# Kernel optimization log

Hardware: AMD Instinct MI355X
Metric: run time of the kernel (lower is better)

The kernel has to match this reference:

```python
import jax, jax.numpy as jnp
import numpy as np
import itertools

GRID_SIZES = [0.01, 0.02, 0.04, 0.08, 0.16, 0.32, 0.64, 1.28]
OFFSETS = np.array(list(itertools.product([-1, 0, 1], repeat=3)), dtype=np.int32)  # [27,3]; index 13 = (0,0,0)
B, N, IN_DIM, HID, OUT_DIM = 2, 65536, 3, 32, 128


def make_neighbors(p, g):
    """Submanifold-conv neighbor tables for one grid scale.
    Returns nbr [27, b*n] int32 (flat point id or -1) and mask [27, b*n] bool.
    """
    b, n, _ = p.shape
    D = int(np.ceil(1.0 / g)) + 1  # static upper bound on spatial shape (p in [0,1))
    gc = jnp.floor(p / g).astype(jnp.int32)
    gc = gc - jnp.min(gc, axis=1, keepdims=True)  # per-batch min, as in torch code
    ids = jnp.arange(b * n, dtype=jnp.int32).reshape(b, n)
    bidx = jnp.arange(b, dtype=jnp.int32)[:, None]
    # deterministic voxel hash: one representative point id per occupied voxel
    grid = jnp.full((b, D, D, D), -1, jnp.int32)
    grid = grid.at[bidx, gc[..., 0], gc[..., 1], gc[..., 2]].max(ids)
    off = jnp.asarray(OFFSETS)
    nc = gc[None] + off[:, None, None, :]  # [27,b,n,3]
    valid = jnp.all((nc >= 0) & (nc < D), axis=-1)
    ncc = jnp.clip(nc, 0, D - 1)
    nbr = grid[bidx[None], ncc[..., 0], ncc[..., 1], ncc[..., 2]]  # [27,b,n]
    mask = valid & (nbr >= 0)
    nbr = nbr.at[13].set(ids)  # center tap is always the point itself
    mask = mask.at[13].set(True)
    return nbr.reshape(27, b * n), mask.reshape(27, b * n)


def subm_conv(f, W, bias, nbr, mask):
    """Submanifold 3x3x3 sparse conv on active sites.
    f [M,h]; W [27,h,h]; nbr/mask [27,M]. out[p] = bias + sum_k (f @ W_k)[nbr_k(p)] (masked).
    Scan over the 27 kernel taps keeps peak memory at O(M*h).
    """
    def step(acc, kin):
        Wk, nbrk, mk = kin
        acc = acc + jnp.where(mk[:, None], (f @ Wk)[nbrk], 0.0)
        return acc, None
    acc0 = jnp.zeros_like(f) + bias
    out, _ = jax.lax.scan(step, acc0, (W, nbr, mask))
    return out


def mssc_forward(p, w1, b1, w_mlp, b_mlp, w_conv, b_conv, w2, b2, neighbors):
    b, n, _ = p.shape
    pts = p @ w1 + b1  # mlp_1: [b,n,HID]
    outs = []
    for i in range(len(GRID_SIZES)):
        nbr, mask = neighbors[i]
        h0 = (pts @ w_mlp[i] + b_mlp[i]).reshape(b * n, HID)  # per-scale MLP
        h1 = subm_conv(h0, w_conv[2 * i], b_conv[2 * i], nbr, mask) + h0
        h2 = subm_conv(h1, w_conv[2 * i + 1], b_conv[2 * i + 1], nbr, mask) + h1
        outs.append(h2 + h0)  # features + features_batch residual
    feat = jnp.concatenate(outs, axis=1).reshape(b, n, HID * len(GRID_SIZES))
    return feat @ w2 + b2  # mlp_2


def setup_inputs():
    key = jax.random.key(0)
    ks = jax.random.split(key, 10)
    L = len(GRID_SIZES)
    return {
        "p": jax.random.uniform(ks[0], (B, N, IN_DIM), jnp.float32),
        "w1": jax.random.normal(ks[1], (IN_DIM, HID), jnp.float32) / np.sqrt(IN_DIM),
        "b1": 0.01 * jax.random.normal(ks[2], (HID,), jnp.float32),
        "w_mlp": jax.random.normal(ks[3], (L, HID, HID), jnp.float32) / np.sqrt(HID),
        "b_mlp": 0.01 * jax.random.normal(ks[4], (L, HID), jnp.float32),
        "w_conv": jax.random.normal(ks[5], (2 * L, 27, HID, HID), jnp.float32) / np.sqrt(27 * HID),
        "b_conv": 0.01 * jax.random.normal(ks[6], (2 * L, HID), jnp.float32),
        "w2": jax.random.normal(ks[7], (HID * L, OUT_DIM), jnp.float32) / np.sqrt(HID * L),
        "b2": 0.01 * jax.random.normal(ks[8], (OUT_DIM,), jnp.float32),
    }


def reference(p, w1, b1, w_mlp, b_mlp, w_conv, b_conv, w2, b2):
    neighbors = [make_neighbors(p, g) for g in GRID_SIZES]
    return mssc_forward(p, w1, b1, w_mlp, b_mlp, w_conv, b_conv, w2, b2, neighbors)
```

## Files before the change

### kernel.cpp

```cpp
#include <hip/hip_runtime.h>

#define MTOT 131072
#define NB   65536
#define SNBINS 265302
#define SNB_BLOCKS 1037

typedef __attribute__((ext_vector_type(8))) __bf16 bf16x8;
typedef __attribute__((ext_vector_type(4))) __bf16 bf16x4;
typedef __attribute__((ext_vector_type(4))) float  f32x4;

__global__ void pmin_init_kernel(float* pmin){
    if (threadIdx.x < 6) pmin[threadIdx.x] = 2.0f;
}

__global__ void pmin_kernel(const float* __restrict__ p, float* __restrict__ pmin){
    int bi = blockIdx.y;
    float m0 = 2.f, m1 = 2.f, m2 = 2.f;
    for (int ni = blockIdx.x * blockDim.x + threadIdx.x; ni < NB; ni += gridDim.x * blockDim.x){
        const float* pp = p + ((size_t)bi * NB + ni) * 3;
        m0 = fminf(m0, pp[0]); m1 = fminf(m1, pp[1]); m2 = fminf(m2, pp[2]);
    }
    #pragma unroll
    for (int o = 32; o > 0; o >>= 1){
        m0 = fminf(m0, __shfl_down(m0, o, 64));
        m1 = fminf(m1, __shfl_down(m1, o, 64));
        m2 = fminf(m2, __shfl_down(m2, o, 64));
    }
    if ((threadIdx.x & 63) == 0){
        atomicMin((int*)(pmin + bi*3 + 0), __float_as_int(m0));
        atomicMin((int*)(pmin + bi*3 + 1), __float_as_int(m1));
        atomicMin((int*)(pmin + bi*3 + 2), __float_as_int(m2));
    }
}

__device__ __forceinline__ int sort_bin(const float* __restrict__ p, int m){
    int bi = m >> 16;
    int gx = (int)(p[m*3+0] * 51.0f); gx = gx > 50 ? 50 : gx;
    int gy = (int)(p[m*3+1] * 51.0f); gy = gy > 50 ? 50 : gy;
    int gz = (int)(p[m*3+2] * 51.0f); gz = gz > 50 ? 50 : gz;
    return bi * 132651 + (gx * 51 + gy) * 51 + gz;
}

__global__ void shist_kernel(const float* __restrict__ p, int* __restrict__ hist){
    int m = blockIdx.x * 256 + threadIdx.x;
    atomicAdd(hist + sort_bin(p, m), 1);
}

__global__ void sscan1_kernel(const int* __restrict__ hist, int* __restrict__ offs,
                              int* __restrict__ bsum){
    __shared__ int sh[256];
    int tid = threadIdx.x;
    int idx = blockIdx.x * 256 + tid;
    int v = (idx < SNBINS) ? hist[idx] : 0;
    sh[tid] = v;
    __syncthreads();
    #pragma unroll
    for (int off = 1; off < 256; off <<= 1){
        int t = (tid >= off) ? sh[tid - off] : 0;
        __syncthreads();
        sh[tid] += t;
        __syncthreads();
    }
    if (idx < SNBINS) offs[idx] = sh[tid] - v;
    if (tid == 255) bsum[blockIdx.x] = sh[255];
}

__global__ void sscan2_kernel(int* __restrict__ bsum){
    __shared__ int sh[256];
    int tid = threadIdx.x;
    const int CH = (SNB_BLOCKS + 255) / 256;
    int base = tid * CH, sum = 0;
    #pragma unroll
    for (int i = 0; i < CH; i++){
        int idx = base + i;
        if (idx < SNB_BLOCKS) sum += bsum[idx];
    }
    sh[tid] = sum;
    __syncthreads();
    #pragma unroll
    for (int off = 1; off < 256; off <<= 1){
        int t = (tid >= off) ? sh[tid - off] : 0;
        __syncthreads();
        sh[tid] += t;
        __syncthreads();
    }
    int run = (tid == 0) ? 0 : sh[tid - 1];
    #pragma unroll
    for (int i = 0; i < CH; i++){
        int idx = base + i;
        if (idx < SNB_BLOCKS){ int v = bsum[idx]; bsum[idx] = run; run += v; }
    }
}

__global__ void sscan3_kernel(int* __restrict__ offs, const int* __restrict__ bsum){
    int idx = blockIdx.x * 256 + threadIdx.x;
    if (idx < SNBINS) offs[idx] += bsum[blockIdx.x];
}

__global__ void sscatter_kernel(const float* __restrict__ p, int* __restrict__ offs,
                                int* __restrict__ sortpos, int* __restrict__ origid){
    int m = blockIdx.x * 256 + threadIdx.x;
    int pos = atomicAdd(offs + sort_bin(p, m), 1);
    sortpos[m] = pos;
    origid[pos] = m;
}

template<int USE_LDS>
__global__ void scatter_kernel(const float* __restrict__ p, const float* __restrict__ pmin,
                               int* __restrict__ vgrid, int* __restrict__ gcbuf,
                               double gd, int D){
    extern __shared__ int lgrid[];
    int m  = blockIdx.x * blockDim.x + threadIdx.x;
    int bi = m >> 16;
    double px = (double)p[m*3], py = (double)p[m*3+1], pz = (double)p[m*3+2];
    int gx = (int)floor(px / gd) - (int)floor((double)pmin[bi*3+0] / gd);
    int gy = (int)floor(py / gd) - (int)floor((double)pmin[bi*3+1] / gd);
    int gz = (int)floor(pz / gd) - (int)floor((double)pmin[bi*3+2] / gd);
    gcbuf[m] = (gx << 20) | (gy << 10) | gz;
    int cell = (gx * D + gy) * D + gz;

    if (!USE_LDS){
        atomicMax(vgrid + bi * D * D * D + cell, m);
        return;
    }
    int ncell = D * D * D;
    for (int c = threadIdx.x; c < ncell; c += 256) lgrid[c] = -1;
    __syncthreads();
    atomicMax(&lgrid[cell], m);
    __syncthreads();
    int* vg = vgrid + bi * ncell;
    for (int c = threadIdx.x; c < ncell; c += 256){
        int v = lgrid[c];
        if (v >= 0) atomicMax(vg + c, v);
    }
}

__global__ void nbr_kernel(const int* __restrict__ gcbuf, const int* __restrict__ vgrid,
                           const int* __restrict__ origid, const int* __restrict__ sortpos,
                           int* __restrict__ nbr, int D){
    int s  = blockIdx.x * blockDim.x + threadIdx.x;
    int m  = origid ? origid[s] : s;
    int bi = m >> 16;
    int pk = gcbuf[m];
    int gx = pk >> 20, gy = (pk >> 10) & 1023, gz = pk & 1023;
    #pragma unroll
    for (int k = 0; k < 27; k++){
        int v;
        if (k == 13){
            v = s;
        } else {
            int x = gx + (k/9) - 1;
            int y = gy + ((k/3)%3) - 1;
            int z = gz + (k%3) - 1;
            if (x < 0 || y < 0 || z < 0 || x >= D || y >= D || z >= D) v = -1;
            else {
                v = vgrid[((bi * D + x) * D + y) * D + z];
                if (v >= 0 && sortpos) v = sortpos[v];
            }
        }
        nbr[k * MTOT + s] = v;
    }
}

__global__ void nbrv_kernel(const int* __restrict__ vgrid, const int* __restrict__ sortpos,
                            int* __restrict__ nbrv, int D, int NC2, int NC2pad){
    int ci = blockIdx.x * 256 + threadIdx.x;
    if (ci >= NC2pad) return;
    int D3 = D * D * D;
    int bi = (ci >= D3) ? 1 : 0;
    int r  = ci - bi * D3;
    int x = r / (D*D), y = (r / D) % D, z = r % D;
    #pragma unroll
    for (int k = 0; k < 27; k++){
        int v = -1;
        if (ci < NC2){
            int nx = x + (k/9) - 1;
            int ny = y + ((k/3)%3) - 1;
            int nz = z + (k%3) - 1;
            if (nx >= 0 && ny >= 0 && nz >= 0 && nx < D && ny < D && nz < D){
                v = vgrid[bi * D3 + ((nx * D + ny) * D + nz)];
                if (v >= 0 && sortpos) v = sortpos[v];
            }
        }
        nbrv[k * NC2pad + ci] = v;
    }
}

__global__ void wcv_wave_kernel(const float* __restrict__ w_conv,
                                __bf16* __restrict__ wth, __bf16* __restrict__ wtl){
    int o = blockIdx.x * 256 + threadIdx.x;
    int cv = o / 27648, r = o % 27648;
    int k = r / 1024, q = r % 1024;
    int half = q >> 9, t = q & 511;
    int l = t >> 3, e = t & 7;
    int c = half*16 + (l & 15);
    int j = (l >> 4)*8 + e;
    float x = w_conv[cv*27648 + k*1024 + j*32 + c];
    __bf16 hi = (__bf16)x;
    wth[o] = hi;
    wtl[o] = (__bf16)(x - (float)hi);
}

__global__ void wcv_kernel(const float* __restrict__ w_conv,
                           __bf16* __restrict__ wth, __bf16* __restrict__ wtl){
    int o = blockIdx.x * 256 + threadIdx.x;
    int cv = o / 27648, r = o % 27648;
    int k = r / 1024, q = r % 1024, c = q / 32, j = q % 32;
    float x = w_conv[cv*27648 + k*1024 + j*32 + c];
    __bf16 hi = (__bf16)x;
    wth[o] = hi;
    wtl[o] = (__bf16)(x - (float)hi);
}

__global__ void w2t_kernel(const float* __restrict__ w2,
                           __bf16* __restrict__ w2th, __bf16* __restrict__ w2tl){
    int o = blockIdx.x * 256 + threadIdx.x;
    int kc = o >> 12, r = o & 4095, c = r >> 5, j = r & 31;
    float x = w2[(kc*32 + j)*128 + c];
    __bf16 hi = (__bf16)x;
    w2th[o] = hi;
    w2tl[o] = (__bf16)(x - (float)hi);
}

__global__ void mlp_scale_kernel(const float* __restrict__ p, const int* __restrict__ origid,
                                 const float* __restrict__ w1, const float* __restrict__ b1,
                                 const float* __restrict__ w, const float* __restrict__ b,
                                 __bf16* __restrict__ h0h, __bf16* __restrict__ h0l){
    int t = blockIdx.x * blockDim.x + threadIdx.x;
    int c = t & 31, s = t >> 5;
    int m = origid ? origid[s] : s;
    float x = p[m*3+0], y = p[m*3+1], z = p[m*3+2];
    float acc = b[c];
    #pragma unroll
    for (int j = 0; j < 32; j++){
        float ptsj = b1[j] + x * w1[j] + y * w1[32 + j] + z * w1[64 + j];
        acc += ptsj * w[j*32 + c];
    }
    __bf16 hi = (__bf16)acc;
    h0h[t] = hi;
    h0l[t] = (__bf16)(acc - (float)hi);
}

template<int MODE>
__global__ __launch_bounds__(256)
void conv4_kernel(const __bf16* __restrict__ fh, const __bf16* __restrict__ fl,
                  const __bf16* __restrict__ wth, const __bf16* __restrict__ wtl,
                  const float* __restrict__ bias, const int* __restrict__ nbr,
                  const __bf16* __restrict__ r2h, const __bf16* __restrict__ r2l,
                  __bf16* __restrict__ outh, __bf16* __restrict__ outl)
{
    __shared__ float buf0[32][33], buf1[32][33];
    int tid  = threadIdx.x;
    int lane = tid & 63, w = tid >> 6;
    int col  = lane & 15, kq = lane >> 4;
    int ptA  = blockIdx.x * 32 + col, ptB = ptA + 16;
    const int fragoff = kq * 8;

    f32x4 acc00, acc01, acc10, acc11;
    if (w == 0){
        float bv0 = bias[col], bv1 = bias[col + 16];
        acc00 = (f32x4){bv0,bv0,bv0,bv0}; acc01 = (f32x4){bv1,bv1,bv1,bv1};
        acc10 = (f32x4){bv0,bv0,bv0,bv0}; acc11 = (f32x4){bv1,bv1,bv1,bv1};
    } else {
        acc00 = (f32x4){0,0,0,0}; acc01 = (f32x4){0,0,0,0};
        acc10 = (f32x4){0,0,0,0}; acc11 = (f32x4){0,0,0,0};
    }

    int k0 = w * 7, k1 = (k0 + 7 < 27) ? k0 + 7 : 27;

    int idc = nbr[k0 * MTOT + ptA];
    int jdc = nbr[k0 * MTOT + ptB];
    int idn = (k0 + 1 < k1) ? nbr[(k0+1) * MTOT + ptA] : 0;
    int jdn = (k0 + 1 < k1) ? nbr[(k0+1) * MTOT + ptB] : 0;
    size_t oc0 = (size_t)(idc < 0 ? 0 : idc) * 32 + fragoff;
    size_t oc1 = (size_t)(jdc < 0 ? 0 : jdc) * 32 + fragoff;
    bf16x8 a0h = *(const bf16x8*)(fh + oc0);
    bf16x8 a0l = *(const bf16x8*)(fl + oc0);
    bf16x8 a1h = *(const bf16x8*)(fh + oc1);
    bf16x8 a1l = *(const bf16x8*)(fl + oc1);
    bool mc0 = idc < 0, mc1 = jdc < 0;

    #pragma unroll 1
    for (int k = k0; k < k1; k++){
        int idn2 = 0, jdn2 = 0;
        if (k + 2 < k1){ idn2 = nbr[(k+2) * MTOT + ptA]; jdn2 = nbr[(k+2) * MTOT + ptB]; }
        size_t on0 = (size_t)(idn < 0 ? 0 : idn) * 32 + fragoff;
        size_t on1 = (size_t)(jdn < 0 ? 0 : jdn) * 32 + fragoff;
        bf16x8 na0h = *(const bf16x8*)(fh + on0);
        bf16x8 na0l = *(const bf16x8*)(fl + on0);
        bf16x8 na1h = *(const bf16x8*)(fh + on1);
        bf16x8 na1l = *(const bf16x8*)(fl + on1);
        bool nm0 = idn < 0, nm1 = jdn < 0;

        const __bf16* wb = wth + (size_t)k*1024 + lane*8;
        const __bf16* wc = wtl + (size_t)k*1024 + lane*8;
        bf16x8 b0h = *(const bf16x8*)(wb);
        bf16x8 b1h = *(const bf16x8*)(wb + 512);
        bf16x8 b0l = *(const bf16x8*)(wc);
        bf16x8 b1l = *(const bf16x8*)(wc + 512);

        bf16x8 z = {};
        bf16x8 xa0h = mc0 ? z : a0h, xa0l = mc0 ? z : a0l;
        bf16x8 xa1h = mc1 ? z : a1h, xa1l = mc1 ? z : a1l;

        acc00 = __builtin_amdgcn_mfma_f32_16x16x32_bf16(xa0h, b0h, acc00, 0,0,0);
        acc00 = __builtin_amdgcn_mfma_f32_16x16x32_bf16(xa0h, b0l, acc00, 0,0,0);
        acc00 = __builtin_amdgcn_mfma_f32_16x16x32_bf16(xa0l, b0h, acc00, 0,0,0);
        acc01 = __builtin_amdgcn_mfma_f32_16x16x32_bf16(xa0h, b1h, acc01, 0,0,0);
        acc01 = __builtin_amdgcn_mfma_f32_16x16x32_bf16(xa0h, b1l, acc01, 0,0,0);
        acc01 = __builtin_amdgcn_mfma_f32_16x16x32_bf16(xa0l, b1h, acc01, 0,0,0);
        acc10 = __builtin_amdgcn_mfma_f32_16x16x32_bf16(xa1h, b0h, acc10, 0,0,0);
        acc10 = __builtin_amdgcn_mfma_f32_16x16x32_bf16(xa1h, b0l, acc10, 0,0,0);
        acc10 = __builtin_amdgcn_mfma_f32_16x16x32_bf16(xa1l, b0h, acc10, 0,0,0);
        acc11 = __builtin_amdgcn_mfma_f32_16x16x32_bf16(xa1h, b1h, acc11, 0,0,0);
// ... 154 lines not shown
        acc00 = __builtin_amdgcn_mfma_f32_16x16x32_bf16(xa0h, b0h, acc00, 0,0,0);
        acc00 = __builtin_amdgcn_mfma_f32_16x16x32_bf16(xa0h, b0l, acc00, 0,0,0);
        acc00 = __builtin_amdgcn_mfma_f32_16x16x32_bf16(xa0l, b0h, acc00, 0,0,0);
        acc01 = __builtin_amdgcn_mfma_f32_16x16x32_bf16(xa0h, b1h, acc01, 0,0,0);
        acc01 = __builtin_amdgcn_mfma_f32_16x16x32_bf16(xa0h, b1l, acc01, 0,0,0);
        acc01 = __builtin_amdgcn_mfma_f32_16x16x32_bf16(xa0l, b1h, acc01, 0,0,0);
        acc10 = __builtin_amdgcn_mfma_f32_16x16x32_bf16(xa1h, b0h, acc10, 0,0,0);
        acc10 = __builtin_amdgcn_mfma_f32_16x16x32_bf16(xa1h, b0l, acc10, 0,0,0);
        acc10 = __builtin_amdgcn_mfma_f32_16x16x32_bf16(xa1l, b0h, acc10, 0,0,0);
        acc11 = __builtin_amdgcn_mfma_f32_16x16x32_bf16(xa1h, b1h, acc11, 0,0,0);
        acc11 = __builtin_amdgcn_mfma_f32_16x16x32_bf16(xa1h, b1l, acc11, 0,0,0);
        acc11 = __builtin_amdgcn_mfma_f32_16x16x32_bf16(xa1l, b1h, acc11, 0,0,0);

        a0h = na0h; a0l = na0l; a1h = na1h; a1l = na1l;
        mc0 = nm0; mc1 = nm1; idn = idn2; jdn = jdn2;
    }

    if (w == 2){
        #pragma unroll
        for (int r = 0; r < 4; r++){
            buf0[kq*4 + r][col]           = acc00[r];
            buf0[kq*4 + r][col + 16]      = acc01[r];
            buf0[16 + kq*4 + r][col]      = acc10[r];
            buf0[16 + kq*4 + r][col + 16] = acc11[r];
        }
    } else if (w == 3){
        #pragma unroll
        for (int r = 0; r < 4; r++){
            buf1[kq*4 + r][col]           = acc00[r];
            buf1[kq*4 + r][col + 16]      = acc01[r];
            buf1[16 + kq*4 + r][col]      = acc10[r];
            buf1[16 + kq*4 + r][col + 16] = acc11[r];
        }
    }
    __syncthreads();
    if (w == 0){
        #pragma unroll
        for (int r = 0; r < 4; r++){
            acc00[r] += buf0[kq*4 + r][col];
            acc01[r] += buf0[kq*4 + r][col + 16];
            acc10[r] += buf0[16 + kq*4 + r][col];
            acc11[r] += buf0[16 + kq*4 + r][col + 16];
        }
    } else if (w == 1){
        #pragma unroll
        for (int r = 0; r < 4; r++){
            acc00[r] += buf1[kq*4 + r][col];
            acc01[r] += buf1[kq*4 + r][col + 16];
            acc10[r] += buf1[16 + kq*4 + r][col];
            acc11[r] += buf1[16 + kq*4 + r][col + 16];
        }
    }
    __syncthreads();
    if (w == 1){
        #pragma unroll
        for (int r = 0; r < 4; r++){
            buf1[kq*4 + r][col]           = acc00[r];
            buf1[kq*4 + r][col + 16]      = acc01[r];
            buf1[16 + kq*4 + r][col]      = acc10[r];
            buf1[16 + kq*4 + r][col + 16] = acc11[r];
        }
    }
    __syncthreads();
    if (w == 0){
        #pragma unroll
        for (int r = 0; r < 4; r++){
            buf0[kq*4 + r][col]           = acc00[r] + buf1[kq*4 + r][col];
            buf0[kq*4 + r][col + 16]      = acc01[r] + buf1[kq*4 + r][col + 16];
            buf0[16 + kq*4 + r][col]      = acc10[r] + buf1[16 + kq*4 + r][col];
            buf0[16 + kq*4 + r][col + 16] = acc11[r] + buf1[16 + kq*4 + r][col + 16];
        }
    }
    __syncthreads();

    int pt = tid >> 3, c0 = (tid & 7) * 4;
    float* o = vv + (size_t)(blockIdx.x * 32 + pt) * 32 + c0;
    ((float4*)o)[0] = make_float4(buf0[pt][c0], buf0[pt][c0+1], buf0[pt][c0+2], buf0[pt][c0+3]);
}

template<int MODE>
__global__ __launch_bounds__(256)
void combine_kernel(const __bf16* __restrict__ fh, const __bf16* __restrict__ fl,
                    const __bf16* __restrict__ wth, const __bf16* __restrict__ wtl,
                    const float* __restrict__ vv, const int* __restrict__ gcbuf,
                    const int* __restrict__ origid, int D,
                    const __bf16* __restrict__ r2h, const __bf16* __restrict__ r2l,
                    __bf16* __restrict__ outh, __bf16* __restrict__ outl)
{
    __shared__ float vsh[128][33];
    int tid  = threadIdx.x;
    int lane = tid & 63, w = tid >> 6;
    int col  = lane & 15, kq = lane >> 4;
    const int fragoff = kq * 8;
    int mB  = blockIdx.x * 128 + w * 32;
    int ptA = mB + col, ptB = ptA + 16;

    size_t oA = (size_t)ptA * 32 + fragoff;
    size_t oB = (size_t)ptB * 32 + fragoff;
    bf16x8 a0h = *(const bf16x8*)(fh + oA);
    bf16x8 a0l = *(const bf16x8*)(fl + oA);
    bf16x8 a1h = *(const bf16x8*)(fh + oB);
    bf16x8 a1l = *(const bf16x8*)(fl + oB);

    const __bf16* wb = wth + 13*1024 + lane*8;
    const __bf16* wc = wtl + 13*1024 + lane*8;
    bf16x8 b0h = *(const bf16x8*)(wb);
    bf16x8 b1h = *(const bf16x8*)(wb + 512);
    bf16x8 b0l = *(const bf16x8*)(wc);
    bf16x8 b1l = *(const bf16x8*)(wc + 512);

    f32x4 acc00 = {0,0,0,0}, acc01 = {0,0,0,0}, acc10 = {0,0,0,0}, acc11 = {0,0,0,0};
    acc00 = __builtin_amdgcn_mfma_f32_16x16x32_bf16(a0h, b0h, acc00, 0,0,0);
    acc00 = __builtin_amdgcn_mfma_f32_16x16x32_bf16(a0h, b0l, acc00, 0,0,0);
    acc00 = __builtin_amdgcn_mfma_f32_16x16x32_bf16(a0l, b0h, acc00, 0,0,0);
    acc01 = __builtin_amdgcn_mfma_f32_16x16x32_bf16(a0h, b1h, acc01, 0,0,0);
    acc01 = __builtin_amdgcn_mfma_f32_16x16x32_bf16(a0h, b1l, acc01, 0,0,0);
    acc01 = __builtin_amdgcn_mfma_f32_16x16x32_bf16(a0l, b1h, acc01, 0,0,0);
    acc10 = __builtin_amdgcn_mfma_f32_16x16x32_bf16(a1h, b0h, acc10, 0,0,0);
    acc10 = __builtin_amdgcn_mfma_f32_16x16x32_bf16(a1h, b0l, acc10, 0,0,0);
    acc10 = __builtin_amdgcn_mfma_f32_16x16x32_bf16(a1l, b0h, acc10, 0,0,0);
    acc11 = __builtin_amdgcn_mfma_f32_16x16x32_bf16(a1h, b1h, acc11, 0,0,0);
    acc11 = __builtin_amdgcn_mfma_f32_16x16x32_bf16(a1h, b1l, acc11, 0,0,0);
    acc11 = __builtin_amdgcn_mfma_f32_16x16x32_bf16(a1l, b1h, acc11, 0,0,0);

    #pragma unroll
    for (int r = 0; r < 4; r++){
        vsh[w*32 + kq*4 + r][col]           = acc00[r];
        vsh[w*32 + kq*4 + r][col + 16]      = acc01[r];
        vsh[w*32 + 16 + kq*4 + r][col]      = acc10[r];
        vsh[w*32 + 16 + kq*4 + r][col + 16] = acc11[r];
    }
    __syncthreads();

    int pt = tid >> 1, c0 = (tid & 1) * 16;
    int s  = blockIdx.x * 128 + pt;
    int m  = origid ? origid[s] : s;
    int pk = gcbuf[m];
    int bi = m >> 16;
    int gx = pk >> 20, gy = (pk >> 10) & 1023, gz = pk & 1023;
    int ci = ((bi * D + gx) * D + gy) * D + gz;

    const float* vrow = vv + (size_t)ci * 32 + c0;
    size_t g = (size_t)s * 32 + c0;
    bf16x8 rh0 = *(const bf16x8*)(fh + g);
    bf16x8 rh1 = *(const bf16x8*)(fh + g + 8);
    bf16x8 rl0 = *(const bf16x8*)(fl + g);
    bf16x8 rl1 = *(const bf16x8*)(fl + g + 8);
    bf16x8 sh0, sh1, sl0, sl1;
    if (MODE == 1){
        sh0 = *(const bf16x8*)(r2h + g);
        sh1 = *(const bf16x8*)(r2h + g + 8);
        sl0 = *(const bf16x8*)(r2l + g);
        sl1 = *(const bf16x8*)(r2l + g + 8);
    }
    bf16x8 oh0, oh1, ol0, ol1;
    #pragma unroll
    for (int j = 0; j < 8; j++){
        float v = vsh[pt][c0 + j] + vrow[j] + (float)rh0[j] + (float)rl0[j];
        if (MODE == 1) v += (float)sh0[j] + (float)sl0[j];
        __bf16 hi = (__bf16)v;
        oh0[j] = hi; ol0[j] = (__bf16)(v - (float)hi);
    }
    #pragma unroll
    for (int j = 0; j < 8; j++){
        float v = vsh[pt][c0 + 8 + j] + vrow[8 + j] + (float)rh1[j] + (float)rl1[j];
        if (MODE == 1) v += (float)sh1[j] + (float)sl1[j];
        __bf16 hi = (__bf16)v;
        oh1[j] = hi; ol1[j] = (__bf16)(v - (float)hi);
    }
    *(bf16x8*)(outh + g)     = oh0;
    *(bf16x8*)(outh + g + 8) = oh1;
    *(bf16x8*)(outl + g)     = ol0;
    *(bf16x8*)(outl + g + 8) = ol1;
}

__global__ __launch_bounds__(256)
void mlp2_kernel(const __bf16* __restrict__ vplanes,
                 const __bf16* __restrict__ w2th, const __bf16* __restrict__ w2tl,
                 const float* __restrict__ b2, const int* __restrict__ origid,
                 float* __restrict__ out)
{
    int tid  = threadIdx.x;
    int lane = tid & 63, w = tid >> 6;
    int col  = lane & 15, kq = lane >> 4;
    const int fragoff = kq * 8;
    int pbase = blockIdx.x * 128 + w * 32;
    size_t oA = (size_t)(pbase + col) * 32 + fragoff;
    size_t oB = (size_t)(pbase + 16 + col) * 32 + fragoff;

    f32x4 acc[4][4];
    #pragma unroll
    for (int s = 0; s < 4; s++)
        #pragma unroll
        for (int q = 0; q < 4; q++) acc[s][q] = (f32x4){0,0,0,0};

    bf16x8 a0h = *(const bf16x8*)(vplanes + oA);
    bf16x8 a0l = *(const bf16x8*)(vplanes + 4194304 + oA);
    bf16x8 a1h = *(const bf16x8*)(vplanes + oB);
    bf16x8 a1l = *(const bf16x8*)(vplanes + 4194304 + oB);

    #pragma unroll 1
    for (int kc = 0; kc < 8; kc++){
        bf16x8 na0h, na0l, na1h, na1l;
        if (kc < 7){
            const __bf16* fnh = vplanes + (size_t)(kc+1) * 8388608;
            const __bf16* fnl = fnh + 4194304;
            na0h = *(const bf16x8*)(fnh + oA);
            na0l = *(const bf16x8*)(fnl + oA);
            na1h = *(const bf16x8*)(fnh + oB);
            na1l = *(const bf16x8*)(fnl + oB);
        } else {
            na0h = a0h; na0l = a0l; na1h = a1h; na1l = a1l;
        }

        const __bf16* wbase  = w2th + (size_t)kc * 4096;
        const __bf16* wlbase = w2tl + (size_t)kc * 4096;
        #pragma unroll
        for (int s = 0; s < 4; s++){
            const __bf16* wb = wbase  + (s*32 + col) * 32 + fragoff;
            const __bf16* wc = wlbase + (s*32 + col) * 32 + fragoff;
            bf16x8 b0h = *(const bf16x8*)(wb);
            bf16x8 b1h = *(const bf16x8*)(wb + 512);
            bf16x8 b0l = *(const bf16x8*)(wc);
            bf16x8 b1l = *(const bf16x8*)(wc + 512);

            acc[s][0] = __builtin_amdgcn_mfma_f32_16x16x32_bf16(a0h, b0h, acc[s][0], 0,0,0);
            acc[s][0] = __builtin_amdgcn_mfma_f32_16x16x32_bf16(a0h, b0l, acc[s][0], 0,0,0);
            acc[s][0] = __builtin_amdgcn_mfma_f32_16x16x32_bf16(a0l, b0h, acc[s][0], 0,0,0);
            acc[s][1] = __builtin_amdgcn_mfma_f32_16x16x32_bf16(a0h, b1h, acc[s][1], 0,0,0);
            acc[s][1] = __builtin_amdgcn_mfma_f32_16x16x32_bf16(a0h, b1l, acc[s][1], 0,0,0);
            acc[s][1] = __builtin_amdgcn_mfma_f32_16x16x32_bf16(a0l, b1h, acc[s][1], 0,0,0);
            acc[s][2] = __builtin_amdgcn_mfma_f32_16x16x32_bf16(a1h, b0h, acc[s][2], 0,0,0);
            acc[s][2] = __builtin_amdgcn_mfma_f32_16x16x32_bf16(a1h, b0l, acc[s][2], 0,0,0);
            acc[s][2] = __builtin_amdgcn_mfma_f32_16x16x32_bf16(a1l, b0h, acc[s][2], 0,0,0);
            acc[s][3] = __builtin_amdgcn_mfma_f32_16x16x32_bf16(a1h, b1h, acc[s][3], 0,0,0);
            acc[s][3] = __builtin_amdgcn_mfma_f32_16x16x32_bf16(a1h, b1l, acc[s][3], 0,0,0);
            acc[s][3] = __builtin_amdgcn_mfma_f32_16x16x32_bf16(a1l, b1h, acc[s][3], 0,0,0);
        }

        a0h = na0h; a0l = na0l; a1h = na1h; a1l = na1l;
    }

    #pragma unroll
    for (int s = 0; s < 4; s++){
        float bl = b2[s*32 + col], bh = b2[s*32 + 16 + col];
        #pragma unroll
        for (int r = 0; r < 4; r++){
            int iA = pbase + kq*4 + r;
            int iB = pbase + 16 + kq*4 + r;
            size_t rowA = (size_t)(origid ? origid[iA] : iA) * 128;
            size_t rowB = (size_t)(origid ? origid[iB] : iB) * 128;
            out[rowA + s*32 + col]      = acc[s][0][r] + bl;
            out[rowA + s*32 + 16 + col] = acc[s][1][r] + bh;
            out[rowB + s*32 + col]      = acc[s][2][r] + bl;
            out[rowB + s*32 + 16 + col] = acc[s][3][r] + bh;
        }
    }
}

template<int MODE>
__global__ __launch_bounds__(256)
void conv_mfma_kernel(const __bf16* __restrict__ fh, const __bf16* __restrict__ fl,
                      const __bf16* __restrict__ wth, const __bf16* __restrict__ wtl,
                      const float* __restrict__ bias, const int* __restrict__ nbr,
                      const __bf16* __restrict__ r2h, const __bf16* __restrict__ r2l,
                      const float* __restrict__ w2i, const float* __restrict__ b2,
                      __bf16* __restrict__ outh, __bf16* __restrict__ outl,
                      float* __restrict__ out)
{
    __shared__ float vsh[64][33];
    int tid  = threadIdx.x;
    int lane = tid & 63, wid = tid >> 6;
    int pair = wid >> 1;
    int half = wid & 1;
    int col  = lane & 15, kq = lane >> 4;
    int m0   = blockIdx.x * 64 + pair * 32;
    int ptA  = m0 + col, ptB = ptA + 16;
    const int fragoff = kq * 8;

    f32x4 acc00, acc01, acc10, acc11;
    if (half == 0){
        float bv0 = bias[col], bv1 = bias[col + 16];
        acc00 = (f32x4){bv0,bv0,bv0,bv0}; acc01 = (f32x4){bv1,bv1,bv1,bv1};
        acc10 = (f32x4){bv0,bv0,bv0,bv0}; acc11 = (f32x4){bv1,bv1,bv1,bv1};
    } else {
        acc00 = (f32x4){0,0,0,0}; acc01 = (f32x4){0,0,0,0};
        acc10 = (f32x4){0,0,0,0}; acc11 = (f32x4){0,0,0,0};
    }

    int k0 = half ? 14 : 0;
    int k1 = half ? 27 : 14;
    #pragma unroll 1
    for (int k = k0; k < k1; k++){
        int nb0 = nbr[k * MTOT + ptA];
        int nb1 = nbr[k * MTOT + ptB];
        size_t o0 = (size_t)(nb0 < 0 ? 0 : nb0) * 32 + fragoff;
        size_t o1 = (size_t)(nb1 < 0 ? 0 : nb1) * 32 + fragoff;
        bf16x8 a0h = *(const bf16x8*)(fh + o0);
        bf16x8 a0l = *(const bf16x8*)(fl + o0);
        bf16x8 a1h = *(const bf16x8*)(fh + o1);
        bf16x8 a1l = *(const bf16x8*)(fl + o1);
        bf16x8 z = {};
        if (nb0 < 0){ a0h = z; a0l = z; }
        if (nb1 < 0){ a1h = z; a1l = z; }

        const __bf16* wb = wth + (size_t)k*1024 + col*32 + fragoff;
        const __bf16* wc = wtl + (size_t)k*1024 + col*32 + fragoff;
        bf16x8 b0h = *(const bf16x8*)(wb);
        bf16x8 b1h = *(const bf16x8*)(wb + 512);
        bf16x8 b0l = *(const bf16x8*)(wc);
        bf16x8 b1l = *(const bf16x8*)(wc + 512);

        acc00 = __builtin_amdgcn_mfma_f32_16x16x32_bf16(a0h, b0h, acc00, 0,0,0);
        acc00 = __builtin_amdgcn_mfma_f32_16x16x32_bf16(a0h, b0l, acc00, 0,0,0);
        acc00 = __builtin_amdgcn_mfma_f32_16x16x32_bf16(a0l, b0h, acc00, 0,0,0);
        acc01 = __builtin_amdgcn_mfma_f32_16x16x32_bf16(a0h, b1h, acc01, 0,0,0);
        acc01 = __builtin_amdgcn_mfma_f32_16x16x32_bf16(a0h, b1l, acc01, 0,0,0);
        acc01 = __builtin_amdgcn_mfma_f32_16x16x32_bf16(a0l, b1h, acc01, 0,0,0);
        acc10 = __builtin_amdgcn_mfma_f32_16x16x32_bf16(a1h, b0h, acc10, 0,0,0);
        acc10 = __builtin_amdgcn_mfma_f32_16x16x32_bf16(a1h, b0l, acc10, 0,0,0);
        acc10 = __builtin_amdgcn_mfma_f32_16x16x32_bf16(a1l, b0h, acc10, 0,0,0);
        acc11 = __builtin_amdgcn_mfma_f32_16x16x32_bf16(a1h, b1h, acc11, 0,0,0);
        acc11 = __builtin_amdgcn_mfma_f32_16x16x32_bf16(a1h, b1l, acc11, 0,0,0);
        acc11 = __builtin_amdgcn_mfma_f32_16x16x32_bf16(a1l, b1h, acc11, 0,0,0);
    }

    if (half == 1){
        #pragma unroll
        for (int r = 0; r < 4; r++){
            vsh[pair*32 + kq*4 + r][col]           = acc00[r];
            vsh[pair*32 + kq*4 + r][col + 16]      = acc01[r];
            vsh[pair*32 + 16 + kq*4 + r][col]      = acc10[r];
            vsh[pair*32 + 16 + kq*4 + r][col + 16] = acc11[r];
        }
    }
    __syncthreads();
    if (half == 0){
        #pragma unroll
// ... 20 lines not shown
            oh8[j] = hi;
            ol8[j] = (__bf16)(v - (float)hi);
        }
        *(bf16x8*)(outh + g) = oh8;
        *(bf16x8*)(outl + g) = ol8;
    } else {
        int eidx = tid * 8;
        int pt = eidx >> 5, c0 = eidx & 31;
        size_t g = (size_t)blockIdx.x * 2048 + eidx;
        bf16x8 rh = *(const bf16x8*)(fh + g);
        bf16x8 rl = *(const bf16x8*)(fl + g);
        bf16x8 sh = *(const bf16x8*)(r2h + g);
        bf16x8 sl = *(const bf16x8*)(r2l + g);
        #pragma unroll
        for (int j = 0; j < 8; j++)
            vsh[pt][c0 + j] += (float)rh[j] + (float)rl[j] + (float)sh[j] + (float)sl[j];
        __syncthreads();

        int pm = tid & 63;
        int tg = __builtin_amdgcn_readfirstlane(tid >> 6);
        size_t m = (size_t)blockIdx.x * 64 + pm;
        float o32[32];
        float* obase = out + m*128 + tg*32;
        if (MODE == 2){
            #pragma unroll
            for (int o = 0; o < 32; o++) o32[o] = b2[tg*32 + o];
        } else {
            #pragma unroll
            for (int q = 0; q < 8; q++){
                float4 t4 = ((const float4*)obase)[q];
                o32[q*4+0] = t4.x; o32[q*4+1] = t4.y; o32[q*4+2] = t4.z; o32[q*4+3] = t4.w;
            }
        }
        #pragma unroll
        for (int c = 0; c < 32; c++){
            float vc = vsh[pm][c];
            const float* w2r = w2i + c*128 + tg*32;
            #pragma unroll
            for (int o = 0; o < 32; o++) o32[o] += vc * w2r[o];
        }
        #pragma unroll
        for (int q = 0; q < 8; q++)
            ((float4*)obase)[q] = make_float4(o32[q*4+0], o32[q*4+1], o32[q*4+2], o32[q*4+3]);
    }
}

extern "C" void kernel_launch(void* const* d_in, const int* in_sizes, int n_in,
                              void* d_out, int out_size, void* d_ws, size_t ws_size,
                              hipStream_t stream)
{
    static const int want[9] = {393216, 96, 32, 8192, 256, 442368, 512, 32768, 128};
    const void* bound[9];
    for (int i = 0; i < 9; i++) bound[i] = d_in[i];
    if (n_in == 9){
        for (int i = 0; i < 9; i++)
            for (int j = 0; j < 9; j++)
                if (in_sizes[j] == want[i]) { bound[i] = d_in[j]; break; }
    }
    const float* p      = (const float*)bound[0];
    const float* w1     = (const float*)bound[1];
    const float* b1     = (const float*)bound[2];
    const float* w_mlp  = (const float*)bound[3];
    const float* b_mlp  = (const float*)bound[4];
    const float* w_conv = (const float*)bound[5];
    const float* b_conv = (const float*)bound[6];
    const float* w2     = (const float*)bound[7];
    const float* b2     = (const float*)bound[8];
    float* out = (float*)d_out;

    char* ws = (char*)d_ws;
    __bf16* h0h  = (__bf16*)(ws);
    __bf16* h0l  = (__bf16*)(ws + 8388608);
    __bf16* h1h  = (__bf16*)(ws + 16777216);
    int*    vgrid= (int*)   (ws + 16777216);
    __bf16* h1l  = (__bf16*)(ws + 25165824);
    int*    nbr  = (int*)   (ws + 33554432);
    int*    nbrv = (int*)   (ws + 33554432);
    float*  vv   = (float*) (ws + 33554432 + 6291456);
    __bf16* wth  = (__bf16*)(ws + 47710208);
    __bf16* wtl  = (__bf16*)(ws + 48594944);
    __bf16* w2th = (__bf16*)(ws + 49479680);
    __bf16* w2tl = (__bf16*)(ws + 49545216);
    float*  pmin = (float*) (ws + 49610752);
    int*    gcbuf= (int*)   (ws + 49612800);
    __bf16* vpl  = (__bf16*)(ws + 50331648);
    int*    hist = (int*)   (ws + 184549376);
    int*    offs = (int*)   (ws + 185614336);
    int*    sortpos=(int*)  (ws + 186679296);
    int*    origid =(int*)  (ws + 187203584);
    int*    bsum   =(int*)  (ws + 187727872);

    const bool big = (ws_size >= 184549376ULL);
    const bool srt = (ws_size >= 187736064ULL);
    const int* oid = srt ? origid  : nullptr;
    const int* spp = srt ? sortpos : nullptr;

    static const double GS[8] = {0.01, 0.02, 0.04, 0.08, 0.16, 0.32, 0.64, 1.28};
    static const int    DS[8] = {101, 51, 26, 14, 8, 5, 3, 2};

    pmin_init_kernel<<<1, 64, 0, stream>>>(pmin);
    pmin_kernel<<<dim3(64, 2), 256, 0, stream>>>(p, pmin);
    if (big){
        wcv_wave_kernel<<<1728, 256, 0, stream>>>(w_conv, wth, wtl);
        w2t_kernel<<<128, 256, 0, stream>>>(w2, w2th, w2tl);
    } else {
        wcv_kernel<<<1728, 256, 0, stream>>>(w_conv, wth, wtl);
    }
    if (srt){
        hipMemsetAsync(hist, 0, SNBINS*sizeof(int), stream);
        shist_kernel<<<MTOT/256, 256, 0, stream>>>(p, hist);
        sscan1_kernel<<<SNB_BLOCKS, 256, 0, stream>>>(hist, offs, bsum);
        sscan2_kernel<<<1, 256, 0, stream>>>(bsum);
        sscan3_kernel<<<SNB_BLOCKS, 256, 0, stream>>>(offs, bsum);
        sscatter_kernel<<<MTOT/256, 256, 0, stream>>>(p, offs, sortpos, origid);
    }

    for (int i = 0; i < 8; i++){
        int D = DS[i]; double gd = GS[i];
        int ncell = D * D * D;
        int NC2 = 2 * ncell;
        hipMemsetAsync(vgrid, 0xFF, (size_t)NC2*sizeof(int), stream);
        if (ncell <= 2744)
            scatter_kernel<1><<<MTOT/256, 256, ncell*sizeof(int), stream>>>(p, pmin, vgrid, gcbuf, gd, D);
        else
            scatter_kernel<0><<<MTOT/256, 256, 0, stream>>>(p, pmin, vgrid, gcbuf, gd, D);

        const bool voxel = big && (NC2 < MTOT);

        if (voxel){
            int NC2pad = (NC2 + 31) & ~31;
            nbrv_kernel<<<(NC2pad + 255)/256, 256, 0, stream>>>(vgrid, spp, nbrv, D, NC2, NC2pad);
            mlp_scale_kernel<<<(MTOT*32)/256, 256, 0, stream>>>(
                p, oid, w1, b1, w_mlp + i*1024, b_mlp + i*32, h0h, h0l);
            vconv_kernel<<<NC2pad/32, 256, 0, stream>>>(
                h0h, h0l, wth + (size_t)(2*i)*27648, wtl + (size_t)(2*i)*27648,
                b_conv + (2*i)*32, nbrv, NC2pad, vv);
            combine_kernel<0><<<MTOT/128, 256, 0, stream>>>(
                h0h, h0l, wth + (size_t)(2*i)*27648, wtl + (size_t)(2*i)*27648,
                vv, gcbuf, oid, D, nullptr, nullptr, h1h, h1l);
            vconv_kernel<<<NC2pad/32, 256, 0, stream>>>(
                h1h, h1l, wth + (size_t)(2*i+1)*27648, wtl + (size_t)(2*i+1)*27648,
                b_conv + (2*i+1)*32, nbrv, NC2pad, vv);
            combine_kernel<1><<<MTOT/128, 256, 0, stream>>>(
                h1h, h1l, wth + (size_t)(2*i+1)*27648, wtl + (size_t)(2*i+1)*27648,
                vv, gcbuf, oid, D, h0h, h0l,
                vpl + (size_t)i*8388608, vpl + (size_t)i*8388608 + 4194304);
        } else {
            nbr_kernel<<<MTOT/256, 256, 0, stream>>>(gcbuf, vgrid, oid, spp, nbr, D);
            mlp_scale_kernel<<<(MTOT*32)/256, 256, 0, stream>>>(
                p, oid, w1, b1, w_mlp + i*1024, b_mlp + i*32, h0h, h0l);
            if (big){
                conv4_kernel<0><<<MTOT/32, 256, 0, stream>>>(
                    h0h, h0l, wth + (size_t)(2*i)*27648, wtl + (size_t)(2*i)*27648,
                    b_conv + (2*i)*32, nbr, nullptr, nullptr, h1h, h1l);
                conv4_kernel<1><<<MTOT/32, 256, 0, stream>>>(
                    h1h, h1l, wth + (size_t)(2*i+1)*27648, wtl + (size_t)(2*i+1)*27648,
                    b_conv + (2*i+1)*32, nbr, h0h, h0l,
                    vpl + (size_t)i*8388608, vpl + (size_t)i*8388608 + 4194304);
            } else {
                conv_mfma_kernel<0><<<MTOT/64, 256, 0, stream>>>(
                    h0h, h0l, wth + (size_t)(2*i)*27648, wtl + (size_t)(2*i)*27648,
                    b_conv + (2*i)*32, nbr, nullptr, nullptr, nullptr, nullptr,
                    h1h, h1l, nullptr);
                if (i == 0)
                    conv_mfma_kernel<2><<<MTOT/64, 256, 0, stream>>>(
                        h1h, h1l, wth + (size_t)(2*i+1)*27648, wtl + (size_t)(2*i+1)*27648,
                        b_conv + (2*i+1)*32, nbr, h0h, h0l, w2 + i*32*128, b2,
                        nullptr, nullptr, out);
                else
                    conv_mfma_kernel<1><<<MTOT/64, 256, 0, stream>>>(
                        h1h, h1l, wth + (size_t)(2*i+1)*27648, wtl + (size_t)(2*i+1)*27648,
                        b_conv + (2*i+1)*32, nbr, h0h, h0l, w2 + i*32*128, nullptr,
                        nullptr, nullptr, out);
            }
        }
    }
    if (big)
        mlp2_kernel<<<MTOT/128, 256, 0, stream>>>(vpl, w2th, w2tl, b2, oid, out);
}
```

Measured before the change: 887.2 us.

## Store coordinates and points in sorted order; translate voxel grid once; halve mlp2 tile

Writes the packed voxel coordinates (now carrying the batch bit) and a sorted copy of the point positions directly in sorted order. A small per-scale kernel remaps the voxel grid to sorted ids once, so the neighbor and combine kernels no longer do indirect origid/sortpos lookups per tap. The mlp2 kernel now handles 64 points per block instead of 128, which doubles the grid and lowers register use per wave. This costs an extra pass over the grid at each scale and a larger workspace requirement; if the workspace is too small, the sorted path is disabled.

Result: no change. 900.6 us (+1.5%).

```diff
diff --git a/kernel.cpp b/kernel.cpp
--- a/kernel.cpp
+++ b/kernel.cpp
@@ -98,16 +98,21 @@
 }
 
 __global__ void sscatter_kernel(const float* __restrict__ p, int* __restrict__ offs,
-                                int* __restrict__ sortpos, int* __restrict__ origid){
+                                int* __restrict__ sortpos, int* __restrict__ origid,
+                                float* __restrict__ ps){
     int m = blockIdx.x * 256 + threadIdx.x;
     int pos = atomicAdd(offs + sort_bin(p, m), 1);
     sortpos[m] = pos;
     origid[pos] = m;
+    ps[pos*3+0] = p[m*3+0];
+    ps[pos*3+1] = p[m*3+1];
+    ps[pos*3+2] = p[m*3+2];
 }
 
 template<int USE_LDS>
 __global__ void scatter_kernel(const float* __restrict__ p, const float* __restrict__ pmin,
-                               int* __restrict__ vgrid, int* __restrict__ gcbuf,
+                               const int* __restrict__ sortpos,
+                               int* __restrict__ vgrid, int* __restrict__ gcs,
                                double gd, int D){
     extern __shared__ int lgrid[];
     int m  = blockIdx.x * blockDim.x + threadIdx.x;
@@ -116,7 +121,8 @@
     int gx = (int)floor(px / gd) - (int)floor((double)pmin[bi*3+0] / gd);
     int gy = (int)floor(py / gd) - (int)floor((double)pmin[bi*3+1] / gd);
     int gz = (int)floor(pz / gd) - (int)floor((double)pmin[bi*3+2] / gd);
-    gcbuf[m] = (gx << 20) | (gy << 10) | gz;
+    int pos = sortpos ? sortpos[m] : m;
+    gcs[pos] = (bi << 30) | (gx << 20) | (gy << 10) | gz;
     int cell = (gx * D + gy) * D + gz;
 
     if (!USE_LDS){
@@ -135,14 +141,19 @@
     }
 }
 
-__global__ void nbr_kernel(const int* __restrict__ gcbuf, const int* __restrict__ vgrid,
-                           const int* __restrict__ origid, const int* __restrict__ sortpos,
+__global__ void vgtrans_kernel(int* __restrict__ vgrid, const int* __restrict__ sortpos, int NC2){
+    int c = blockIdx.x * 256 + threadIdx.x;
+    if (c >= NC2) return;
+    int v = vgrid[c];
+    if (v >= 0) vgrid[c] = sortpos[v];
+}
+
+__global__ void nbr_kernel(const int* __restrict__ gcs, const int* __restrict__ vgrid,
                            int* __restrict__ nbr, int D){
     int s  = blockIdx.x * blockDim.x + threadIdx.x;
-    int m  = origid ? origid[s] : s;
-    int bi = m >> 16;
-    int pk = gcbuf[m];
-    int gx = pk >> 20, gy = (pk >> 10) & 1023, gz = pk & 1023;
+    int pk = gcs[s];
+    int bi = (pk >> 30) & 1;
+    int gx = (pk >> 20) & 1023, gy = (pk >> 10) & 1023, gz = pk & 1023;
     #pragma unroll
     for (int k = 0; k < 27; k++){
         int v;
@@ -153,17 +164,14 @@
             int y = gy + ((k/3)%3) - 1;
             int z = gz + (k%3) - 1;
             if (x < 0 || y < 0 || z < 0 || x >= D || y >= D || z >= D) v = -1;
-            else {
-                v = vgrid[((bi * D + x) * D + y) * D + z];
-                if (v >= 0 && sortpos) v = sortpos[v];
-            }
+            else v = vgrid[((bi * D + x) * D + y) * D + z];
         }
         nbr[k * MTOT + s] = v;
     }
 }
 
-__global__ void nbrv_kernel(const int* __restrict__ vgrid, const int* __restrict__ sortpos,
-                            int* __restrict__ nbrv, int D, int NC2, int NC2pad){
+__global__ void nbrv_kernel(const int* __restrict__ vgrid, int* __restrict__ nbrv,
+                            int D, int NC2, int NC2pad){
     int ci = blockIdx.x * 256 + threadIdx.x;
     if (ci >= NC2pad) return;
     int D3 = D * D * D;
@@ -177,10 +185,8 @@
             int nx = x + (k/9) - 1;
             int ny = y + ((k/3)%3) - 1;
             int nz = z + (k%3) - 1;
-            if (nx >= 0 && ny >= 0 && nz >= 0 && nx < D && ny < D && nz < D){
+            if (nx >= 0 && ny >= 0 && nz >= 0 && nx < D && ny < D && nz < D)
                 v = vgrid[bi * D3 + ((nx * D + ny) * D + nz)];
-                if (v >= 0 && sortpos) v = sortpos[v];
-            }
         }
         nbrv[k * NC2pad + ci] = v;
     }
@@ -222,14 +228,13 @@
     w2tl[o] = (__bf16)(x - (float)hi);
 }
 
-__global__ void mlp_scale_kernel(const float* __restrict__ p, const int* __restrict__ origid,
+__global__ void mlp_scale_kernel(const float* __restrict__ pp,
                                  const float* __restrict__ w1, const float* __restrict__ b1,
                                  const float* __restrict__ w, const float* __restrict__ b,
                                  __bf16* __restrict__ h0h, __bf16* __restrict__ h0l){
     int t = blockIdx.x * blockDim.x + threadIdx.x;
     int c = t & 31, s = t >> 5;
-    int m = origid ? origid[s] : s;
-    float x = p[m*3+0], y = p[m*3+1], z = p[m*3+2];
+    float x = pp[s*3+0], y = pp[s*3+1], z = pp[s*3+2];
     float acc = b[c];
     #pragma unroll
     for (int j = 0; j < 32; j++){
@@ -550,8 +555,7 @@
 __global__ __launch_bounds__(256)
 void combine_kernel(const __bf16* __restrict__ fh, const __bf16* __restrict__ fl,
                     const __bf16* __restrict__ wth, const __bf16* __restrict__ wtl,
-                    const float* __restrict__ vv, const int* __restrict__ gcbuf,
-                    const int* __restrict__ origid, int D,
+                    const float* __restrict__ vv, const int* __restrict__ gcs, int D,
                     const __bf16* __restrict__ r2h, const __bf16* __restrict__ r2l,
                     __bf16* __restrict__ outh, __bf16* __restrict__ outl)
 {
@@ -602,10 +606,9 @@
 
     int pt = tid >> 1, c0 = (tid & 1) * 16;
     int s  = blockIdx.x * 128 + pt;
-    int m  = origid ? origid[s] : s;
-    int pk = gcbuf[m];
-    int bi = m >> 16;
-    int gx = pk >> 20, gy = (pk >> 10) & 1023, gz = pk & 1023;
+    int pk = gcs[s];
+    int bi = (pk >> 30) & 1;
+    int gx = (pk >> 20) & 1023, gy = (pk >> 10) & 1023, gz = pk & 1023;
     int ci = ((bi * D + gx) * D + gy) * D + gz;
 
     const float* vrow = vv + (size_t)ci * 32 + c0;
@@ -652,34 +655,27 @@
     int lane = tid & 63, w = tid >> 6;
     int col  = lane & 15, kq = lane >> 4;
     const int fragoff = kq * 8;
-    int pbase = blockIdx.x * 128 + w * 32;
+    int pbase = blockIdx.x * 64 + w * 16;
     size_t oA = (size_t)(pbase + col) * 32 + fragoff;
-    size_t oB = (size_t)(pbase + 16 + col) * 32 + fragoff;
-
-    f32x4 acc[4][4];
-    #pragma unroll
-    for (int s = 0; s < 4; s++)
-        #pragma unroll
-        for (int q = 0; q < 4; q++) acc[s][q] = (f32x4){0,0,0,0};
+
+    f32x4 acc[4][2];
+    #pragma unroll
+    for (int s = 0; s < 4; s++){
+        acc[s][0] = (f32x4){0,0,0,0};
+        acc[s][1] = (f32x4){0,0,0,0};
+    }
 
     bf16x8 a0h = *(const bf16x8*)(vplanes + oA);
     bf16x8 a0l = *(const bf16x8*)(vplanes + 4194304 + oA);
-    bf16x8 a1h = *(const bf16x8*)(vplanes + oB);
-    bf16x8 a1l = *(const bf16x8*)(vplanes + 4194304 + oB);
 
     #pragma unroll 1
     for (int kc = 0; kc < 8; kc++){
-        bf16x8 na0h, na0l, na1h, na1l;
+        bf16x8 na0h, na0l;
         if (kc < 7){
             const __bf16* fnh = vplanes + (size_t)(kc+1) * 8388608;
-            const __bf16* fnl = fnh + 4194304;
             na0h = *(const bf16x8*)(fnh + oA);
-            na0l = *(const bf16x8*)(fnl + oA);
-            na1h = *(const bf16x8*)(fnh + oB);
-            na1l = *(const bf16x8*)(fnl + oB);
-        } else {
-            na0h = a0h; na0l = a0l; na1h = a1h; na1l = a1l;
-        }
+            na0l = *(const bf16x8*)(fnh + 4194304 + oA);
+        } else { na0h = a0h; na0l = a0l; }
 
         const __bf16* wbase  = w2th + (size_t)kc * 4096;
         const __bf16* wlbase = w2tl + (size_t)kc * 4096;
@@ -698,15 +694,9 @@
             acc[s][1] = __builtin_amdgcn_mfma_f32_16x16x32_bf16(a0h, b1h, acc[s][1], 0,0,0);
             acc[s][1] = __builtin_amdgcn_mfma_f32_16x16x32_bf16(a0h, b1l, acc[s][1], 0,0,0);
             acc[s][1] = __builtin_amdgcn_mfma_f32_16x16x32_bf16(a0l, b1h, acc[s][1], 0,0,0);
-            acc[s][2] = __builtin_amdgcn_mfma_f32_16x16x32_bf16(a1h, b0h, acc[s][2], 0,0,0);
-            acc[s][2] = __builtin_amdgcn_mfma_f32_16x16x32_bf16(a1h, b0l, acc[s][2], 0,0,0);
-            acc[s][2] = __builtin_amdgcn_mfma_f32_16x16x32_bf16(a1l, b0h, acc[s][2], 0,0,0);
-            acc[s][3] = __builtin_amdgcn_mfma_f32_16x16x32_bf16(a1h, b1h, acc[s][3], 0,0,0);
-            acc[s][3] = __builtin_amdgcn_mfma_f32_16x16x32_bf16(a1h, b1l, acc[s][3], 0,0,0);
-            acc[s][3] = __builtin_amdgcn_mfma_f32_16x16x32_bf16(a1l, b1h, acc[s][3], 0,0,0);
-        }
-
-        a0h = na0h; a0l = na0l; a1h = na1h; a1l = na1l;
+        }
+
+        a0h = na0h; a0l = na0l;
     }
 
     #pragma unroll
@@ -715,13 +705,9 @@
         #pragma unroll
         for (int r = 0; r < 4; r++){
             int iA = pbase + kq*4 + r;
-            int iB = pbase + 16 + kq*4 + r;
             size_t rowA = (size_t)(origid ? origid[iA] : iA) * 128;
-            size_t rowB = (size_t)(origid ? origid[iB] : iB) * 128;
             out[rowA + s*32 + col]      = acc[s][0][r] + bl;
             out[rowA + s*32 + 16 + col] = acc[s][1][r] + bh;
-            out[rowB + s*32 + col]      = acc[s][2][r] + bl;
-            out[rowB + s*32 + 16 + col] = acc[s][3][r] + bh;
         }
     }
 }
@@ -908,18 +894,20 @@
     __bf16* w2th = (__bf16*)(ws + 49479680);
     __bf16* w2tl = (__bf16*)(ws + 49545216);
     float*  pmin = (float*) (ws + 49610752);
-    int*    gcbuf= (int*)   (ws + 49612800);
+    int*    gcs  = (int*)   (ws + 49612800);
     __bf16* vpl  = (__bf16*)(ws + 50331648);
     int*    hist = (int*)   (ws + 184549376);
     int*    offs = (int*)   (ws + 185614336);
     int*    sortpos=(int*)  (ws + 186679296);
     int*    origid =(int*)  (ws + 187203584);
     int*    bsum   =(int*)  (ws + 187727872);
+    float*  ps     =(float*)(ws + 187736064);
 
     const bool big = (ws_size >= 184549376ULL);
-    const bool srt = (ws_size >= 187736064ULL);
+    const bool srt = (ws_size >= 189308928ULL);
     const int* oid = srt ? origid  : nullptr;
     const int* spp = srt ? sortpos : nullptr;
+    const float* pp = srt ? ps : p;
 
     static const double GS[8] = {0.01, 0.02, 0.04, 0.08, 0.16, 0.32, 0.64, 1.28};
     static const int    DS[8] = {101, 51, 26, 14, 8, 5, 3, 2};
@@ -938,7 +926,7 @@
         sscan1_kernel<<<SNB_BLOCKS, 256, 0, stream>>>(hist, offs, bsum);
         sscan2_kernel<<<1, 256, 0, stream>>>(bsum);
         sscan3_kernel<<<SNB_BLOCKS, 256, 0, stream>>>(offs, bsum);
-        sscatter_kernel<<<MTOT/256, 256, 0, stream>>>(p, offs, sortpos, origid);
+        sscatter_kernel<<<MTOT/256, 256, 0, stream>>>(p, offs, sortpos, origid, ps);
     }
 
     for (int i = 0; i < 8; i++){
@@ -947,34 +935,36 @@
         int NC2 = 2 * ncell;
         hipMemsetAsync(vgrid, 0xFF, (size_t)NC2*sizeof(int), stream);
         if (ncell <= 2744)
-            scatter_kernel<1><<<MTOT/256, 256, ncell*sizeof(int), stream>>>(p, pmin, vgrid, gcbuf, gd, D);
+            scatter_kernel<1><<<MTOT/256, 256, ncell*sizeof(int), stream>>>(p, pmin, spp, vgrid, gcs, gd, D);
         else
-            scatter_kernel<0><<<MTOT/256, 256, 0, stream>>>(p, pmin, vgrid, gcbuf, gd, D);
+            scatter_kernel<0><<<MTOT/256, 256, 0, stream>>>(p, pmin, spp, vgrid, gcs, gd, D);
+        if (srt)
+            vgtrans_kernel<<<(NC2 + 255)/256, 256, 0, stream>>>(vgrid, sortpos, NC2);
 
         const bool voxel = big && (NC2 < MTOT);
 
         if (voxel){
             int NC2pad = (NC2 + 31) & ~31;
-            nbrv_kernel<<<(NC2pad + 255)/256, 256, 0, stream>>>(vgrid, spp, nbrv, D, NC2, NC2pad);
+            nbrv_kernel<<<(NC2pad + 255)/256, 256, 0, stream>>>(vgrid, nbrv, D, NC2, NC2pad);
             mlp_scale_kernel<<<(MTOT*32)/256, 256, 0, stream>>>(
-                p, oid, w1, b1, w_mlp + i*1024, b_mlp + i*32, h0h, h0l);
+                pp, w1, b1, w_mlp + i*1024, b_mlp + i*32, h0h, h0l);
             vconv_kernel<<<NC2pad/32, 256, 0, stream>>>(
                 h0h, h0l, wth + (size_t)(2*i)*27648, wtl + (size_t)(2*i)*27648,
                 b_conv + (2*i)*32, nbrv, NC2pad, vv);
             combine_kernel<0><<<MTOT/128, 256, 0, stream>>>(
                 h0h, h0l, wth + (size_t)(2*i)*27648, wtl + (size_t)(2*i)*27648,
-                vv, gcbuf, oid, D, nullptr, nullptr, h1h, h1l);
+                vv, gcs, D, nullptr, nullptr, h1h, h1l);
             vconv_kernel<<<NC2pad/32, 256, 0, stream>>>(
                 h1h, h1l, wth + (size_t)(2*i+1)*27648, wtl + (size_t)(2*i+1)*27648,
                 b_conv + (2*i+1)*32, nbrv, NC2pad, vv);
             combine_kernel<1><<<MTOT/128, 256, 0, stream>>>(
                 h1h, h1l, wth + (size_t)(2*i+1)*27648, wtl + (size_t)(2*i+1)*27648,
-                vv, gcbuf, oid, D, h0h, h0l,
+                vv, gcs, D, h0h, h0l,
                 vpl + (size_t)i*8388608, vpl + (size_t)i*8388608 + 4194304);
         } else {
-            nbr_kernel<<<MTOT/256, 256, 0, stream>>>(gcbuf, vgrid, oid, spp, nbr, D);
+            nbr_kernel<<<MTOT/256, 256, 0, stream>>>(gcs, vgrid, nbr, D);
             mlp_scale_kernel<<<(MTOT*32)/256, 256, 0, stream>>>(
-                p, oid, w1, b1, w_mlp + i*1024, b_mlp + i*32, h0h, h0l);
+                pp, w1, b1, w_mlp + i*1024, b_mlp + i*32, h0h, h0l);
             if (big){
                 conv4_kernel<0><<<MTOT/32, 256, 0, stream>>>(
                     h0h, h0l, wth + (size_t)(2*i)*27648, wtl + (size_t)(2*i)*27648,
@@ -1002,5 +992,5 @@
         }
     }
     if (big)
-        mlp2_kernel<<<MTOT/128, 256, 0, stream>>>(vpl, w2th, w2tl, b2, oid, out);
-}
+        mlp2_kernel<<<MTOT/64, 256, 0, stream>>>(vpl, w2th, w2tl, b2, oid, out);
+}
```
